# Kernel optimization log

Hardware: AMD Instinct MI355X
Metric: run time of the kernel (lower is better)

The kernel has to match this reference:

```python
import math
import jax, jax.numpy as jnp
import numpy as np

BLOCK = 32          # hard-coded in the CUDA kernels
NUM_HEADS = 16
NUM_BLOCKS = 512    # (max_pos//32) * block_per_row = 128 * 4
DIAG_N = 3
FIRST_N = 0


def _mra2_attention(Q, K, V, mask):
    # Q,K,V: (meta_batch, seq, head_dim); mask: (meta_batch, seq) in {0,1}
    mb, seq_len, d = Q.shape
    bs = BLOCK
    nb = seq_len // bs
    scale = 1.0 / math.sqrt(d)
    Q = Q * mask[:, :, None]
    K = K * mask[:, :, None]
    V = V * mask[:, :, None]

    # ---- low resolution block means (mask-weighted), approx_mode='full' keeps V_hat
    tc = mask.reshape(mb, nb, bs).sum(-1)                 # token count per block
    denom = tc[:, :, None] + 1e-6
    Q_hat = Q.reshape(mb, nb, bs, d).sum(2) / denom       # (mb, nb, d)
    K_hat = K.reshape(mb, nb, bs, d).sum(2) / denom
    V_hat = V.reshape(mb, nb, bs, d).sum(2) / denom
    low_logit = jnp.einsum('bid,bjd->bij', Q_hat, K_hat) * scale
    row_max = low_logit.max(-1, keepdims=True)            # before mask subtraction
    low_logit = low_logit - 10000.0 * ((tc[:, None, :] * tc[:, :, None]) < 0.5).astype(Q.dtype)

    # ---- block index selection (torch runs this under no_grad)
    lrn = jax.lax.stop_gradient(low_logit - row_max)
    if DIAG_N > 0:
        off = DIAG_N // 2
        i = jnp.arange(nb)
        band = (jnp.abs(i[:, None] - i[None, :]) <= off).astype(Q.dtype)
        lrn = lrn + band[None] * 5000.0
    if FIRST_N > 0:
        lrn = lrn.at[:, :FIRST_N, :].add(5000.0)
        lrn = lrn.at[:, :, :FIRST_N].add(5000.0)
    top_vals, indices = jax.lax.top_k(lrn.reshape(mb, nb * nb), NUM_BLOCKS)
    threshold = top_vals.min(-1)
    high_mask = (lrn >= threshold[:, None, None]).astype(Q.dtype)  # selected-block mask

    q_blk = indices // nb                                  # (mb, n) query block ids
    k_blk = indices % nb                                   # (mb, n) key block ids
    Qs = jnp.take_along_axis(Q.reshape(mb, nb, bs, d), q_blk[:, :, None, None], axis=1)
    Ks = jnp.take_along_axis(K.reshape(mb, nb, bs, d), k_blk[:, :, None, None], axis=1)
    Vs = jnp.take_along_axis(V.reshape(mb, nb, bs, d), k_blk[:, :, None, None], axis=1)

    # sampled dense-dense: sparse_C[b,n,k,q] (key-in-block, query-in-block layout as in kernel)
    hi_logit = jnp.einsum('bnkd,bnqd->bnkq', Ks, Qs) * scale

    # per query-row max over selected blocks (kernel index_max; constant for grad)
    b_idx = jnp.arange(mb)[:, None]
    blk_max = hi_logit.max(axis=2)                         # (mb, n, bs) max over key axis
    max_blocks = jnp.full((mb, nb, bs), -1e8, Q.dtype).at[b_idx, q_blk].max(blk_max)
    max_blocks = jax.lax.stop_gradient(max_blocks)
    max_vals = max_blocks.reshape(mb, seq_len)
    max_scatter = jnp.take_along_axis(max_blocks, q_blk[:, :, None], axis=1)[:, :, None, :]

    # key-side mask per selected block (sparse_mask_B)
    mask_blk = jnp.take_along_axis(mask.reshape(mb, nb, bs), k_blk[:, :, None], axis=1)
    hi_attn = jnp.exp(hi_logit - max_scatter - 10000.0 * (1.0 - mask_blk[:, :, :, None]))

    # sparse-dense matmul + reduce-sum normalizer, scattered back per query block
    hi_out = jnp.zeros((mb, nb, bs, d), Q.dtype).at[b_idx, q_blk].add(
        jnp.einsum('bnkq,bnkd->bnqd', hi_attn, Vs)).reshape(mb, seq_len, d)
    hi_norm = jnp.zeros((mb, nb, bs), Q.dtype).at[b_idx, q_blk].add(
        hi_attn.sum(axis=2)).reshape(mb, seq_len)

    # ---- low resolution branch, selected blocks suppressed via high_mask
    low_attn = jnp.exp(low_logit - row_max - 10000.0 * high_mask) * tc[:, None, :]
    low_out = jnp.repeat(jnp.einsum('bij,bjd->bid', low_attn, V_hat), bs, axis=1)
    low_norm = jnp.repeat(low_attn.sum(-1), bs, axis=1)

    log_corr = (jnp.repeat(row_max[:, :, 0], bs, axis=1) - max_vals) * mask
    low_corr = jnp.exp(jnp.minimum(log_corr, 0.0))
    hi_corr = jnp.exp(-jnp.maximum(log_corr, 0.0))

    ctx = hi_out * hi_corr[:, :, None] + low_out * low_corr[:, :, None]
    ctx = ctx / (hi_norm * hi_corr + low_norm * low_corr + 1e-6)[:, :, None]
    return ctx * mask[:, :, None]


def _forward(hidden_states, attention_mask, w_q, b_q, w_k, b_k, w_v, b_v):
    b, s, hdim = hidden_states.shape
    h = NUM_HEADS
    dh = hdim // h

    def split_heads(x):
        return x.reshape(b, s, h, dh).transpose(0, 2, 1, 3).reshape(b * h, s, dh)

    q = split_heads(hidden_states @ w_q.T + b_q)
    k = split_heads(hidden_states @ w_k.T + b_k)
    v = split_heads(hidden_states @ w_v.T + b_v)
    # invert extended additive mask (1 + am/10000) and replicate over heads
    # (torch's .repeat(1, h, 1).reshape(b*h, s) stacks h copies of the [b,s] mask)
    mask = jnp.tile(1.0 + attention_mask / 10000.0, (h, 1))
    ctx = _mra2_attention(q, k, v, mask)
    ctx = ctx.reshape(b, h, s, dh).transpose(0, 2, 1, 3).reshape(b, s, hdim)
    return ctx


def setup_inputs() -> dict:
    key = jax.random.key(0)
    ks = jax.random.split(key, 4)
    H = 1024
    return {
        'hidden_states': jax.random.normal(ks[0], (2, 4096, H), jnp.float32),
        'attention_mask': jnp.zeros((2, 4096), jnp.float32),
        'w_q': jax.random.normal(ks[1], (H, H), jnp.float32) * 0.02,
        'b_q': jnp.zeros((H,), jnp.float32),
        'w_k': jax.random.normal(ks[2], (H, H), jnp.float32) * 0.02,
        'b_k': jnp.zeros((H,), jnp.float32),
        'w_v': jax.random.normal(ks[3], (H, H), jnp.float32) * 0.02,
        'b_v': jnp.zeros((H,), jnp.float32),
    }


def reference(hidden_states, attention_mask, w_q, b_q, w_k, b_k, w_v, b_v):
    return _forward(hidden_states, attention_mask, w_q, b_q, w_k, b_k, w_v, b_v)
```

## Files before the change

kernel.cpp:

```cpp
#include <hip/hip_runtime.h>
#include <cstdint>
#include <cstddef>

#define MAXSEL 160
static constexpr int S    = 4096;
static constexpr int H    = 1024;
static constexpr int DH   = 64;
static constexpr int NB   = 128;
static constexpr int MBH  = 32;
static constexpr int M8   = 8192;
static constexpr int N3   = 3072;

typedef _Float16 half8 __attribute__((ext_vector_type(8)));
typedef _Float16 half4v __attribute__((ext_vector_type(4)));
typedef float floatx4 __attribute__((ext_vector_type(4)));

__device__ __forceinline__ void load_lds16(const void* g, void* l) {
  __builtin_amdgcn_global_load_lds((const __attribute__((address_space(1))) unsigned int*)g,
                                   (__attribute__((address_space(3))) unsigned int*)l,
                                   16, 0, 0);
}

__device__ __forceinline__ int sel8(int t, int4 a, int4 b) {
  int r = a.x;
  r = (t == 1) ? a.y : r;
  r = (t == 2) ? a.z : r;
  r = (t == 3) ? a.w : r;
  r = (t == 4) ? b.x : r;
  r = (t == 5) ? b.y : r;
  r = (t == 6) ? b.z : r;
  r = (t == 7) ? b.w : r;
  return r;
}

__global__ __launch_bounds__(256) void k_prep(const float* __restrict__ hidden,
                                              const float* __restrict__ am,
                                              const float* __restrict__ wq,
                                              const float* __restrict__ wk,
                                              const float* __restrict__ wv,
                                              _Float16* __restrict__ h16,
                                              _Float16* __restrict__ w16,
                                              _Float16* __restrict__ wlo,
                                              _Float16* __restrict__ hb_hi,
                                              _Float16* __restrict__ hb_lo,
                                              float* __restrict__ tcv,
                                              int* __restrict__ selcnt) {
  const int blk_id = blockIdx.x;
  if (blk_id < 256) {
    if (blk_id == 0) {
      for (int i = threadIdx.x; i < MBH * NB; i += 256) selcnt[i] = 0;
    }
    int b2 = blk_id >> 7, blk = blk_id & 127;
    int c = threadIdx.x * 4;
    float4 s0 = make_float4(0.f, 0.f, 0.f, 0.f);
    float4 s1 = make_float4(0.f, 0.f, 0.f, 0.f);
    for (int i = 0; i < 32; i += 4) {
      int pos0 = blk * 32 + i;
      size_t base = ((size_t)b2 * 4096 + pos0) * 1024 + c;
      const float4 x0 = *(const float4*)&hidden[base];
      const float4 x1 = *(const float4*)&hidden[base + 1024];
      const float4 x2 = *(const float4*)&hidden[base + 2048];
      const float4 x3 = *(const float4*)&hidden[base + 3072];
      float a00 = am[pos0],      a01 = am[pos0 + 1],      a02 = am[pos0 + 2],      a03 = am[pos0 + 3];
      float a10 = am[4096+pos0], a11 = am[4096+pos0 + 1], a12 = am[4096+pos0 + 2], a13 = am[4096+pos0 + 3];
      half4v h;
      h[0]=(_Float16)x0.x; h[1]=(_Float16)x0.y; h[2]=(_Float16)x0.z; h[3]=(_Float16)x0.w;
      *(half4v*)&h16[base] = h;
      h[0]=(_Float16)x1.x; h[1]=(_Float16)x1.y; h[2]=(_Float16)x1.z; h[3]=(_Float16)x1.w;
      *(half4v*)&h16[base + 1024] = h;
      h[0]=(_Float16)x2.x; h[1]=(_Float16)x2.y; h[2]=(_Float16)x2.z; h[3]=(_Float16)x2.w;
      *(half4v*)&h16[base + 2048] = h;
      h[0]=(_Float16)x3.x; h[1]=(_Float16)x3.y; h[2]=(_Float16)x3.z; h[3]=(_Float16)x3.w;
      *(half4v*)&h16[base + 3072] = h;
      float m0, m1;
      m0 = 1.f + a00 * 1e-4f; m1 = 1.f + a10 * 1e-4f;
      s0.x += m0*x0.x; s0.y += m0*x0.y; s0.z += m0*x0.z; s0.w += m0*x0.w;
      s1.x += m1*x0.x; s1.y += m1*x0.y; s1.z += m1*x0.z; s1.w += m1*x0.w;
      m0 = 1.f + a01 * 1e-4f; m1 = 1.f + a11 * 1e-4f;
      s0.x += m0*x1.x; s0.y += m0*x1.y; s0.z += m0*x1.z; s0.w += m0*x1.w;
      s1.x += m1*x1.x; s1.y += m1*x1.y; s1.z += m1*x1.z; s1.w += m1*x1.w;
      m0 = 1.f + a02 * 1e-4f; m1 = 1.f + a12 * 1e-4f;
      s0.x += m0*x2.x; s0.y += m0*x2.y; s0.z += m0*x2.z; s0.w += m0*x2.w;
      s1.x += m1*x2.x; s1.y += m1*x2.y; s1.z += m1*x2.z; s1.w += m1*x2.w;
      m0 = 1.f + a03 * 1e-4f; m1 = 1.f + a13 * 1e-4f;
      s0.x += m0*x3.x; s0.y += m0*x3.y; s0.z += m0*x3.z; s0.w += m0*x3.w;
      s1.x += m1*x3.x; s1.y += m1*x3.y; s1.z += m1*x3.z; s1.w += m1*x3.w;
    }
    size_t row0 = (size_t)(b2 * 2 + 0) * 128 + blk;
    size_t row1 = (size_t)(b2 * 2 + 1) * 128 + blk;
    half4v hi, lo;
    hi[0]=(_Float16)s0.x; lo[0]=(_Float16)(s0.x-(float)hi[0]);
    hi[1]=(_Float16)s0.y; lo[1]=(_Float16)(s0.y-(float)hi[1]);
    hi[2]=(_Float16)s0.z; lo[2]=(_Float16)(s0.z-(float)hi[2]);
    hi[3]=(_Float16)s0.w; lo[3]=(_Float16)(s0.w-(float)hi[3]);
    *(half4v*)&hb_hi[row0 * 1024 + c] = hi;
    *(half4v*)&hb_lo[row0 * 1024 + c] = lo;
    hi[0]=(_Float16)s1.x; lo[0]=(_Float16)(s1.x-(float)hi[0]);
    hi[1]=(_Float16)s1.y; lo[1]=(_Float16)(s1.y-(float)hi[1]);
    hi[2]=(_Float16)s1.z; lo[2]=(_Float16)(s1.z-(float)hi[2]);
    hi[3]=(_Float16)s1.w; lo[3]=(_Float16)(s1.w-(float)hi[3]);
    *(half4v*)&hb_hi[row1 * 1024 + c] = hi;
    *(half4v*)&hb_lo[row1 * 1024 + c] = lo;
    if (b2 == 0 && threadIdx.x == 0) {
      float t0 = 0.f, t1 = 0.f;
      for (int i = 0; i < 32; ++i) {
        int pos = blk * 32 + i;
        t0 += 1.f + am[pos] * 1e-4f;
        t1 += 1.f + am[4096 + pos] * 1e-4f;
      }
      tcv[blk] = t0; tcv[128 + blk] = t1;
    }
  } else {
    long j = (long)(blk_id - 256) * 256 + threadIdx.x;
    const long NW4 = (long)H * H / 4;
    int which = (int)(j / NW4);
    long jj = j - (long)which * NW4;
    const float* src = which == 0 ? wq : (which == 1 ? wk : wv);
    float4 x = ((const float4*)src)[jj];
    half4v h;
    h[0] = (_Float16)x.x; h[1] = (_Float16)x.y;
    h[2] = (_Float16)x.z; h[3] = (_Float16)x.w;
    *(half4v*)&w16[j * 4] = h;
    if (which < 2) {
      half4v r;
      r[0] = (_Float16)(x.x - (float)h[0]);
      r[1] = (_Float16)(x.y - (float)h[1]);
      r[2] = (_Float16)(x.z - (float)h[2]);
      r[3] = (_Float16)(x.w - (float)h[3]);
      *(half4v*)&wlo[j * 4] = r;
    }
  }
}

__global__ __launch_bounds__(512, 4) void k_gemm_qkv(const _Float16* __restrict__ A,
                                                     const _Float16* __restrict__ B,
                                                     const float* __restrict__ bq,
                                                     const float* __restrict__ bk,
                                                     const float* __restrict__ bv,
                                                     const float* __restrict__ am,
                                                     _Float16* __restrict__ q16,
                                                     _Float16* __restrict__ k16,
                                                     _Float16* __restrict__ v16,
                                                     const _Float16* __restrict__ Ahi,
                                                     const _Float16* __restrict__ Alo,
                                                     const _Float16* __restrict__ Blo,
                                                     float* __restrict__ sideQK) {
  __shared__ _Float16 sh[36864];

  if (blockIdx.x < 768) {
    const int id = blockIdx.x;
    const int swz = (id & 7) * 96 + (id >> 3);
    const int by = swz / 12;
    const int bx = swz - by * 12;
    const int tid = threadIdx.x;
    const int lane = tid & 63, wv = tid >> 6;
    const int wm = wv >> 2, wn = wv & 3;
    const int l15 = lane & 15, quad = lane >> 4;

    _Float16* As = sh;
    _Float16* Bs = sh + 12288;

    floatx4 acc[4][4] = {};

    const _Float16* Ag = A + (size_t)(by * 128) * 1024;
    const _Float16* Bg = B + (size_t)(bx * 256) * 1024;

    const int gr  = lane >> 2;
    const int gcb = ((lane & 3) ^ ((lane >> 3) & 3)) * 8;
    const _Float16* agl  = Ag + (size_t)(wv * 16 + gr) * 1024 + gcb;
    const _Float16* bgl0 = Bg + (size_t)(wv * 32 + gr) * 1024 + gcb;
    const _Float16* bgl1 = Bg + (size_t)(wv * 32 + 16 + gr) * 1024 + gcb;
    const int aw  = (wv * 16) * 32;
    const int bw0 = (wv * 32) * 32;
    const int bw1 = (wv * 32 + 16) * 32;

#define STAGE(TT, BB)                                                   \
    {                                                                   \
      load_lds16(agl  + (size_t)(TT) * 32, &As[(BB) * 4096 + aw]);      \
      load_lds16(bgl0 + (size_t)(TT) * 32, &Bs[(BB) * 8192 + bw0]);     \
      load_lds16(bgl1 + (size_t)(TT) * 32, &Bs[(BB) * 8192 + bw1]);     \
    }

    STAGE(0, 0)
    STAGE(1, 1)

    const int rc = ((quad ^ ((l15 >> 1) & 3)) << 3);

#pragma unroll
    for (int t = 0; t < 32; ++t) {
      if (t == 31) { asm volatile("s_waitcnt vmcnt(0)" ::: "memory"); }
      else         { asm volatile("s_waitcnt vmcnt(3)" ::: "memory"); }
      __builtin_amdgcn_s_barrier();
      if (t < 30) {
        const int nb = (t + 2) % 3;
        STAGE(t + 2, nb)
      }
      const int bb = t % 3;
      half8 a[4], b[4];
#pragma unroll
      for (int mt = 0; mt < 4; ++mt)
        a[mt] = *(const half8*)&As[bb * 4096 + (wm * 64 + mt * 16 + l15) * 32 + rc];
#pragma unroll
      for (int nt = 0; nt < 4; ++nt)
        b[nt] = *(const half8*)&Bs[bb * 8192 + (wn * 64 + nt * 16 + l15) * 32 + rc];
      __builtin_amdgcn_s_setprio(1);
#pragma unroll
      for (int mt = 0; mt < 4; ++mt)
#pragma unroll
        for (int nt = 0; nt < 4; ++nt)
          acc[mt][nt] = __builtin_amdgcn_mfma_f32_16x16x32_f16(a[mt], b[nt], acc[mt][nt], 0, 0, 0);
      __builtin_amdgcn_s_setprio(0);
    }
#undef STAGE

    const int which = bx >> 2;
    const float* bias = which == 0 ? bq : (which == 1 ? bk : bv);
    _Float16* dst = which == 0 ? q16 : (which == 1 ? k16 : v16);
    const int hh = (bx & 3) * 4 + wn;
    const int m2 = hh & 1;
#pragma unroll
    for (int nt = 0; nt < 4; ++nt) {
      const int dd = nt * 16 + l15;
      const float bsv = bias[hh * 64 + dd];
#pragma unroll
      for (int mt = 0; mt < 4; ++mt) {
#pragma unroll
        for (int r = 0; r < 4; ++r) {
          int srow = by * 128 + wm * 64 + mt * 16 + quad * 4 + r;
          int b2 = srow >> 12, s = srow & 4095;
          float mv = 1.f + am[m2 * 4096 + s] * 1e-4f;
          float v = (acc[mt][nt][r] + bsv) * mv;
          int mb = b2 * 16 + hh;
          dst[((size_t)mb * 4096 + s) * 64 + dd] = (_Float16)v;
        }
      }
    }
    return;
  }

  const int half = threadIdx.x >> 8;
  const int stid = threadIdx.x & 255;
  const int sb   = (blockIdx.x - 768) * 2 + half;
  const int slane = stid & 63, swv = stid >> 6;
  const int kk  = sb >> 8;
  const int sbb = sb & 255;
  const int sbx = sbb & 31;
  const int sby = sbb >> 5;
  const int swm = swv >> 1, swn = swv & 1;
  const int sl15 = slane & 15, squad = slane >> 4;
  _Float16* base = sh + half * 16384;
  _Float16* sAhi = base;
  _Float16* sAlo = base + 4096;
  _Float16* sBhi = base + 8192;
  _Float16* sBlo = base + 12288;

  floatx4 acc[2][2] = {};

  const int srow = slane >> 3;
  const int scol = (((slane & 7) ^ (srow & 7)) * 8);
  const int sswz = sl15 & 7;
  const _Float16* src;
  _Float16* dst;
  if      (swv == 0) { src = Ahi + (size_t)(sby * 64) * 1024; dst = sAhi; }
  else if (swv == 1) { src = Alo + (size_t)(sby * 64) * 1024; dst = sAlo; }
  else if (swv == 2) { src = B   + (size_t)(sbx * 64) * 1024; dst = sBhi; }
  else               { src = Blo + (size_t)(sbx * 64) * 1024; dst = sBlo; }

  const int kbeg = kk * 512;
  for (int k0 = kbeg; k0 < kbeg + 512; k0 += 64) {
    __syncthreads();
#pragma unroll
    for (int i = 0; i < 8; ++i)
      load_lds16(src + (size_t)(i * 8 + srow) * 1024 + k0 + scol, dst + i * 512);
    __syncthreads();
#pragma unroll
    for (int ks = 0; ks < 2; ++ks) {
      const int kc = ks * 4;
      half8 ah[2], al[2], bh[2], bl[2];
#pragma unroll
      for (int mt = 0; mt < 2; ++mt) {
        int off = (swm * 32 + mt * 16 + sl15) * 64 + (((kc + squad) ^ sswz) << 3);
        ah[mt] = *(const half8*)&sAhi[off];
        al[mt] = *(const half8*)&sAlo[off];
      }
#pragma unroll
      for (int nt = 0; nt < 2; ++nt) {
        int off = (swn * 32 + nt * 16 + sl15) * 64 + (((kc + squad) ^ sswz) << 3);
        bh[nt] = *(const half8*)&sBhi[off];
        bl[nt] = *(const half8*)&sBlo[off];
      }
#pragma unroll
      for (int mt = 0; mt < 2; ++mt)
#pragma unroll
        for (int nt = 0; nt < 2; ++nt) {
          acc[mt][nt] = __builtin_amdgcn_mfma_f32_16x16x32_f16(ah[mt], bh[nt], acc[mt][nt], 0, 0, 0);
          acc[mt][nt] = __builtin_amdgcn_mfma_f32_16x16x32_f16(ah[mt], bl[nt], acc[mt][nt], 0, 0, 0);
          acc[mt][nt] = __builtin_amdgcn_mfma_f32_16x16x32_f16(al[mt], bh[nt], acc[mt][nt], 0, 0, 0);
        }
    }
  }
  float* outp = sideQK + (size_t)kk * (512 * 2048);
#pragma unroll
  for (int mt = 0; mt < 2; ++mt)
#pragma unroll
    for (int nt = 0; nt < 2; ++nt)
#pragma unroll
      for (int rr = 0; rr < 4; ++rr) {
        int row = sby * 64 + swm * 32 + mt * 16 + squad * 4 + rr;
        int col = sbx * 64 + swn * 32 + nt * 16 + sl15;
        outp[(size_t)row * 2048 + col] = acc[mt][nt][rr];
      }
}

__global__ __launch_bounds__(256) void k_lowlogit(const float* __restrict__ sideQK,
                                                  const float* __restrict__ tcv,
                                                  const float* __restrict__ bq,
                                                  const float* __restrict__ bk,
                                                  float* __restrict__ ll,
                                                  float* __restrict__ rmaxout,
                                                  const _Float16* __restrict__ v16,
                                                  float* __restrict__ vhat,
                                                  _Float16* __restrict__ v16T) {
  __shared__ __attribute__((aligned(16))) char shraw[37376];
  const int tid = threadIdx.x;

  if (blockIdx.x >= 256) {
    const int lane = tid & 63, wv = tid >> 6;
    _Float16* Vs = (_Float16*)shraw + wv * 2304;
    int bid = (blockIdx.x - 256) * 4 + wv;
    int mb = bid >> 7, blk = bid & 127;
    const _Float16* src = v16 + ((size_t)mb * 4096 + blk * 32) * 64;
    int r = lane >> 3, c = (lane & 7) * 8;
#pragma unroll
    for (int it = 0; it < 4; ++it)
      *(uint4*)&Vs[(it * 8 + r) * 72 + c] = *(const uint4*)&src[(it * 8 + r) * 64 + c];
    __syncthreads();
    float acc = 0.f;
    half8 col[4];
#pragma unroll
    for (int k = 0; k < 32; ++k) {
      _Float16 x = Vs[k * 72 + lane];
      col[k >> 3][k & 7] = x;
      acc += (float)x;
    }
    vhat[(size_t)bid * 64 + lane] = acc / (tcv[(mb & 1) * 128 + blk] + 1e-6f);
    _Float16* dst = v16T + ((size_t)(mb * 128 + blk) * 64 + lane) * 32;
#pragma unroll
    for (int p = 0; p < 4; ++p) *(half8*)&dst[p * 8] = col[p];
    return;
  }

  const int mb = blockIdx.x >> 3;
  const int ib = blockIdx.x & 7;
  const int b2 = mb >> 4, m2 = mb & 1, hh = mb & 15;
  const int combo = b2 * 2 + m2;
  float* Kh  = (float*)shraw;
  float* Qh  = (float*)(shraw + 32768);
  float* tcL = (float*)(shraw + 32768 + 4096);

  const float* P1 = sideQK + (size_t)512 * 2048;

  if (tid < 128) tcL[tid] = tcv[m2 * 128 + tid];
  __syncthreads();
#pragma unroll
  for (int i = 0; i < 8; ++i) {
    int ci = tid + i * 256;
    int row = ci >> 4, c4 = (ci & 15) * 4;
    float tck = tcL[row];
    float den = 1.f / (tck + 1e-6f);
    size_t idx = ((size_t)combo * 128 + row) * 2048 + 1024 + hh * 64 + c4;
    float4 x0 = *(const float4*)&sideQK[idx];
    float4 x1 = *(const float4*)&P1[idx];
    float4 bb = *(const float4*)&bk[hh * 64 + c4];
    float4 o;
    o.x = (x0.x + x1.x + bb.x * tck) * den; o.y = (x0.y + x1.y + bb.y * tck) * den;
    o.z = (x0.z + x1.z + bb.z * tck) * den; o.w = (x0.w + x1.w + bb.w * tck) * den;
    *(float4*)&Kh[row * 64 + c4] = o;
  }
  {
    int row = tid >> 4, c4 = (tid & 15) * 4;
    int gi = ib * 16 + row;
    float tcq = tcL[gi];
    float den = 1.f / (tcq + 1e-6f);
    size_t idx = ((size_t)combo * 128 + gi) * 2048 + hh * 64 + c4;
    float4 x0 = *(const float4*)&sideQK[idx];
    float4 x1 = *(const float4*)&P1[idx];
    float4 bb = *(const float4*)&bq[hh * 64 + c4];
    float4 o;
    o.x = (x0.x + x1.x + bb.x * tcq) * den; o.y = (x0.y + x1.y + bb.y * tcq) * den;
    o.z = (x0.z + x1.z + bb.z * tcq) * den; o.w = (x0.w + x1.w + bb.w * tcq) * den;
    *(float4*)&Qh[row * 64 + c4] = o;
  }
  __syncthreads();

  const int il = tid >> 4, jg = tid & 15;
  const int i = ib * 16 + il;
  float tcq = tcL[i];
  float dots[8] = {};
#pragma unroll
  for (int dd = 0; dd < 16; ++dd) {
    int d4 = ((dd + tid) & 15) * 4;
    float4 qv = *(const float4*)&Qh[il * 64 + d4];
#pragma unroll
    for (int jj = 0; jj < 8; ++jj) {
      float4 kv = *(const float4*)&Kh[(jg * 8 + jj) * 64 + d4];
      dots[jj] += qv.x * kv.x + qv.y * kv.y + qv.z * kv.z + qv.w * kv.w;
    }
  }
  float tmax = -1e30f;
#pragma unroll
  for (int jj = 0; jj < 8; ++jj) {
    int j = jg * 8 + jj;
    float raw = dots[jj] * 0.125f;
    tmax = fmaxf(tmax, raw);
    float pen = (tcq * tcL[j] < 0.5f) ? 10000.f : 0.f;
    ll[(size_t)mb * 16384 + (size_t)i * 128 + j] = raw - pen;
  }
#pragma unroll
  for (int mk = 1; mk < 16; mk <<= 1) tmax = fmaxf(tmax, __shfl_xor(tmax, mk));
  if (jg == 0) rmaxout[mb * 128 + i] = tmax;
}

__global__ __launch_bounds__(256) void k_topk(const float* __restrict__ ll,
                                              const float* __restrict__ rmax,
                                              float* __restrict__ thr,
                                              int* __restrict__ selcnt,
                                              int* __restrict__ selkb) {
  const int mb = blockIdx.x;
  const int t = threadIdx.x;
  const int wid = t >> 6;
  __shared__ int red2[2][4];

  unsigned code[64];
#pragma unroll
  for (int j = 0; j < 64; ++j) {
    int e = j * 256 + t;
    int i = e >> 7, jj = e & 127;
    float lrn = ll[(size_t)mb * 16384 + e] - rmax[mb * 128 + i];
    int di = i - jj;
    if (di <= 1 && di >= -1) lrn += 5000.f;
    unsigned b = __float_as_uint(lrn);
    code[j] = (b & 0x80000000u) ? ~b : (b | 0x80000000u);
  }

  unsigned lo = 0u, hi = 0xFFFFFFFFu;
  for (int it = 0; it < 32; ++it) {
    unsigned mid = lo + ((hi - lo) >> 1);
    int c = 0;
#pragma unroll
    for (int j = 0; j < 64; ++j) c += (code[j] >= mid) ? 1 : 0;
#pragma unroll
    for (int mk = 1; mk < 64; mk <<= 1) c += __shfl_xor(c, mk);
    if ((t & 63) == 0) red2[it & 1][wid] = c;
    __syncthreads();
    int total = red2[it & 1][0] + red2[it & 1][1] + red2[it & 1][2] + red2[it & 1][3];
    if (total >= 512) lo = mid; else hi = mid;
  }
  if (t == 0) {
    unsigned bits = (lo & 0x80000000u) ? (lo & 0x7FFFFFFFu) : ~lo;
    thr[mb] = __uint_as_float(bits);
  }
#pragma unroll
  for (int j = 0; j < 64; ++j) {
    if (code[j] >= lo) {
      int e = j * 256 + t;
      int i = e >> 7, jj = e & 127;
      int slot = atomicAdd(&selcnt[mb * 128 + i], 1);
      if (slot < MAXSEL) selkb[(size_t)(mb * 128 + i) * MAXSEL + slot] = jj;
    }
  }
}

__global__ __launch_bounds__(64) void k_hi(const _Float16* __restrict__ q16,
                                           const _Float16* __restrict__ k16,
                                           const _Float16* __restrict__ v16T,
                                           const int* __restrict__ selcnt,
                                           const int* __restrict__ selkb,
                                           const float* __restrict__ rmax,
                                           const float* __restrict__ thr,
                                           const float* __restrict__ tcv,
                                           const float* __restrict__ vhat,
                                           const float* __restrict__ ll,
                                           const float* __restrict__ am,
                                           float* __restrict__ out) {
  const int mb = blockIdx.x & 31, qb = blockIdx.x >> 5;
  const int sid = mb * 128 + qb;
  const int lane = threadIdx.x;
  const int l15 = lane & 15, quad = lane >> 4;
  const int m2 = mb & 1, b2 = mb >> 4, hh = mb & 15;

  __shared__ _Float16 Ps[32 * 40];

  const _Float16* qbase = q16 + ((size_t)mb * 4096 + qb * 32) * 64;
  half8 aq[2][2];
#pragma unroll
  for (int mt = 0; mt < 2; ++mt)
#pragma unroll
    for (int ks = 0; ks < 2; ++ks)
      aq[mt][ks] = *(const half8*)&qbase[(mt * 16 + l15) * 64 + ks * 32 + quad * 8];

  const int* list = selkb + (size_t)sid * MAXSEL;
  const int4 La = *(const int4*)&list[0];
  const int4 Lb = *(const int4*)&list[4];

  const float rmaxb = rmax[sid];
  const float th = thr[mb];
  const float* llrow = ll + (size_t)mb * 16384 + (size_t)qb * 128;
  const float* tcrow = tcv + m2 * 128;
  const float* vhbase = vhat + ((size_t)(mb * 128)) * 64 + lane;
  float a0 = 0.f, a1 = 0.f, a2 = 0.f, a3 = 0.f;
  float n0 = 0.f, n1 = 0.f, n2 = 0.f, n3 = 0.f;
#pragma unroll 2
  for (int j0 = 0; j0 < 128; j0 += 4) {
    float4 l4 = *(const float4*)&llrow[j0];
    float4 t4 = *(const float4*)&tcrow[j0];
    float v0 = vhbase[(size_t)(j0 + 0) * 64];
    float v1 = vhbase[(size_t)(j0 + 1) * 64];
    float v2 = vhbase[(size_t)(j0 + 2) * 64];
    float v3 = vhbase[(size_t)(j0 + 3) * 64];
    int d0 = qb - j0;
    float lr0 = l4.x - rmaxb + ((d0 <= 1 && d0 >= -1) ? 5000.f : 0.f);
    float lr1 = l4.y - rmaxb + ((d0 <= 2 && d0 >= 0) ? 5000.f : 0.f);
    float lr2 = l4.z - rmaxb + ((d0 <= 3 && d0 >= 1) ? 5000.f : 0.f);
    float lr3 = l4.w - rmaxb + ((d0 <= 4 && d0 >= 2) ? 5000.f : 0.f);
    float w0 = (lr0 >= th) ? 0.f : __expf(l4.x - rmaxb) * t4.x;
    float w1 = (lr1 >= th) ? 0.f : __expf(l4.y - rmaxb) * t4.y;
    float w2 = (lr2 >= th) ? 0.f : __expf(l4.z - rmaxb) * t4.z;
    float w3 = (lr3 >= th) ? 0.f : __expf(l4.w - rmaxb) * t4.w;
    a0 += w0 * v0; a1 += w1 * v1; a2 += w2 * v2; a3 += w3 * v3;
    n0 += w0; n1 += w1; n2 += w2; n3 += w3;
  }
  float accL = (a0 + a1) + (a2 + a3);
  float nrmL = (n0 + n1) + (n2 + n3);

  int nk = selcnt[sid];
  if (nk > MAXSEL) nk = MAXSEL;

  const _Float16* kbase  = k16  + (size_t)mb * 4096 * 64;
  const _Float16* vtbase = v16T + (size_t)mb * 128 * 2048;

  float rm[2][4];
  floatx4 o[2][4] = {};
  floatx4 onrm[2] = {};
#pragma unroll
  for (int mt = 0; mt < 2; ++mt)
#pragma unroll
    for (int r = 0; r < 4; ++r) rm[mt][r] = -1e8f;

  half8 ones;
#pragma unroll
  for (int j = 0; j < 8; ++j) ones[j] = (_Float16)1.f;

  for (int t = 0; t < nk; ++t) {
    const int kb = (t < 8) ? sel8(t, La, Lb) : list[t];
    const _Float16* kp = kbase + (size_t)kb * 32 * 64;
    half8 b0[2], b1[2];
#pragma unroll
    for (int ks = 0; ks < 2; ++ks) {
      b0[ks] = *(const half8*)&kp[(l15) * 64 + ks * 32 + quad * 8];
      b1[ks] = *(const half8*)&kp[(16 + l15) * 64 + ks * 32 + quad * 8];
    }
    const _Float16* vp = vtbase + kb * 2048 + quad * 8;
    half8 vb0 = *(const half8*)&vp[(l15) * 32];
    half8 vb1 = *(const half8*)&vp[(16 + l15) * 32];
    half8 vb2 = *(const half8*)&vp[(32 + l15) * 32];
    half8 vb3 = *(const half8*)&vp[(48 + l15) * 32];

    floatx4 sf[2][2] = {};
    sf[0][0] = __builtin_amdgcn_mfma_f32_16x16x32_f16(aq[0][0], b0[0], sf[0][0], 0, 0, 0);
    sf[0][0] = __builtin_amdgcn_mfma_f32_16x16x32_f16(aq[0][1], b0[1], sf[0][0], 0, 0, 0);
    sf[0][1] = __builtin_amdgcn_mfma_f32_16x16x32_f16(aq[0][0], b1[0], sf[0][1], 0, 0, 0);
    sf[0][1] = __builtin_amdgcn_mfma_f32_16x16x32_f16(aq[0][1], b1[1], sf[0][1], 0, 0, 0);
    sf[1][0] = __builtin_amdgcn_mfma_f32_16x16x32_f16(aq[1][0], b0[0], sf[1][0], 0, 0, 0);
    sf[1][0] = __builtin_amdgcn_mfma_f32_16x16x32_f16(aq[1][1], b0[1], sf[1][0], 0, 0, 0);
    sf[1][1] = __builtin_amdgcn_mfma_f32_16x16x32_f16(aq[1][0], b1[0], sf[1][1], 0, 0, 0);
    sf[1][1] = __builtin_amdgcn_mfma_f32_16x16x32_f16(aq[1][1], b1[1], sf[1][1], 0, 0, 0);

    float pen0, pen1;
    {
      float mk0 = 1.f + am[m2 * 4096 + kb * 32 + l15] * 1e-4f;
      float mk1 = 1.f + am[m2 * 4096 + kb * 32 + 16 + l15] * 1e-4f;
      pen0 = 10000.f * (1.f - mk0);
      pen1 = 10000.f * (1.f - mk1);
    }
#pragma unroll
    for (int mt = 0; mt < 2; ++mt)
#pragma unroll
      for (int r = 0; r < 4; ++r) {
        float s0 = sf[mt][0][r] * 0.125f;
        float s1 = sf[mt][1][r] * 0.125f;
        float v = fmaxf(s0, s1);
#pragma unroll
        for (int mk = 1; mk < 16; mk <<= 1) v = fmaxf(v, __shfl_xor(v, mk));
        float mnew  = fmaxf(rm[mt][r], v);
        float alpha = __expf(rm[mt][r] - mnew);
        rm[mt][r] = mnew;
        float p0 = __expf(s0 - mnew - pen0);
        float p1 = __expf(s1 - mnew - pen1);
        o[mt][0][r] *= alpha; o[mt][1][r] *= alpha;
        o[mt][2][r] *= alpha; o[mt][3][r] *= alpha;
        onrm[mt][r] *= alpha;
        int row = mt * 16 + quad * 4 + r;
        Ps[row * 40 + l15] = (_Float16)p0;
        Ps[row * 40 + 16 + l15] = (_Float16)p1;
      }
    __builtin_amdgcn_sched_barrier(0);
    asm volatile("s_waitcnt lgkmcnt(0)" ::: "memory");
    __builtin_amdgcn_sched_barrier(0);
    half8 pa0 = *(const half8*)&Ps[(l15) * 40 + quad * 8];
    half8 pa1 = *(const half8*)&Ps[(16 + l15) * 40 + quad * 8];
    o[0][0] = __builtin_amdgcn_mfma_f32_16x16x32_f16(pa0, vb0, o[0][0], 0, 0, 0);
    o[0][1] = __builtin_amdgcn_mfma_f32_16x16x32_f16(pa0, vb1, o[0][1], 0, 0, 0);
    o[0][2] = __builtin_amdgcn_mfma_f32_16x16x32_f16(pa0, vb2, o[0][2], 0, 0, 0);
    o[0][3] = __builtin_amdgcn_mfma_f32_16x16x32_f16(pa0, vb3, o[0][3], 0, 0, 0);
    o[1][0] = __builtin_amdgcn_mfma_f32_16x16x32_f16(pa1, vb0, o[1][0], 0, 0, 0);
    o[1][1] = __builtin_amdgcn_mfma_f32_16x16x32_f16(pa1, vb1, o[1][1], 0, 0, 0);
    o[1][2] = __builtin_amdgcn_mfma_f32_16x16x32_f16(pa1, vb2, o[1][2], 0, 0, 0);
    o[1][3] = __builtin_amdgcn_mfma_f32_16x16x32_f16(pa1, vb3, o[1][3], 0, 0, 0);
    onrm[0] = __builtin_amdgcn_mfma_f32_16x16x32_f16(pa0, ones, onrm[0], 0, 0, 0);
    onrm[1] = __builtin_amdgcn_mfma_f32_16x16x32_f16(pa1, ones, onrm[1], 0, 0, 0);
  }

  float lo_d[4];
#pragma unroll
  for (int ntd = 0; ntd < 4; ++ntd) lo_d[ntd] = __shfl(accL, ntd * 16 + l15);
#pragma unroll
  for (int mt = 0; mt < 2; ++mt) {
#pragma unroll
    for (int r = 0; r < 4; ++r) {
      int q = mt * 16 + quad * 4 + r;
      int qpos = qb * 32 + q;
      float mq = 1.f + am[m2 * 4096 + qpos] * 1e-4f;
      float logc = (rmaxb - rm[mt][r]) * mq;
      float lc = __expf(fminf(logc, 0.f));
      float hc = __expf(-fmaxf(logc, 0.f));
      float den = onrm[mt][r] * hc + nrmL * lc + 1e-6f;
      float sc = mq / den;
#pragma unroll
      for (int ntd = 0; ntd < 4; ++ntd) {
        float val = (o[mt][ntd][r] * hc + lo_d[ntd] * lc) * sc;
        out[((size_t)b2 * 4096 + qpos) * 1024 + hh * 64 + ntd * 16 + l15] = val;
      }
    }
  }
}

extern "C" void kernel_launch(void* const* d_in, const int* in_sizes, int n_in,
                              void* d_out, int out_size, void* d_ws, size_t ws_size,
                              hipStream_t stream) {
  const float* hidden = (const float*)d_in[0];
  const float* am     = (const float*)d_in[1];
  const float* wq     = (const float*)d_in[2];
  const float* bq     = (const float*)d_in[3];
  const float* wk     = (const float*)d_in[4];
  const float* bk     = (const float*)d_in[5];
  const float* wv     = (const float*)d_in[6];
  const float* bv     = (const float*)d_in[7];
  float* out = (float*)d_out;

  char* ws = (char*)d_ws;
  size_t off = 0;
  auto alloc = [&](size_t bytes) -> char* {
    char* p = ws + off;
    off += (bytes + 255) & ~(size_t)255;
    return p;
  };
  _Float16* h16    = (_Float16*)alloc((size_t)M8 * H * 2);
  _Float16* w16    = (_Float16*)alloc((size_t)N3 * H * 2);
  _Float16* wlo    = (_Float16*)alloc((size_t)2 * H * H * 2);
  _Float16* q16    = (_Float16*)alloc((size_t)MBH * S * DH * 2);
  _Float16* k16    = (_Float16*)alloc((size_t)MBH * S * DH * 2);
  _Float16* v16    = (_Float16*)alloc((size_t)MBH * S * DH * 2);
  _Float16* hb_hi  = (_Float16*)alloc((size_t)4 * NB * H * 2);
  _Float16* hb_lo  = (_Float16*)alloc((size_t)4 * NB * H * 2);
  float* tcv       = (float*)alloc((size_t)2 * NB * 4);
  float* sideQK    = (float*)alloc((size_t)2 * 512 * 2048 * 4);
  float* ll        = (float*)alloc((size_t)MBH * NB * NB * 4);
  float* rmax      = (float*)alloc((size_t)MBH * NB * 4);
  float* thr       = (float*)alloc((size_t)MBH * 4);
  int*   selcnt    = (int*)alloc((size_t)MBH * NB * 4);
  int*   selkb     = (int*)alloc((size_t)MBH * NB * MAXSEL * 4);
  float* vhat      = (float*)alloc((size_t)MBH * NB * DH * 4);
  _Float16* v16T   = h16;

  k_prep<<<dim3(3328), dim3(256), 0, stream>>>(hidden, am, wq, wk, wv,
                                               h16, w16, wlo, hb_hi, hb_lo, tcv, selcnt);
  k_gemm_qkv<<<dim3(1024), dim3(512), 0, stream>>>(h16, w16, bq, bk, bv, am,
                                                   q16, k16, v16,
                                                   hb_hi, hb_lo, wlo, sideQK);
  k_lowlogit<<<dim3(1280), dim3(256), 0, stream>>>(sideQK, tcv, bq, bk, ll, rmax,
                                                   v16, vhat, v16T);
  k_topk<<<dim3(32), dim3(256), 0, stream>>>(ll, rmax, thr, selcnt, selkb);
  k_hi<<<dim3(4096), dim3(64), 0, stream>>>(q16, k16, v16T, selcnt, selkb, rmax, thr,
                                            tcv, vhat, ll, am, out);
}
```

Baseline: 278.7 us.

## Split k_hi key-block loop across two waves with flash-style merge

k_hi now runs two wavefronts per query block. The waves interleave the selected key blocks and split the low-resolution sweep in half, then merge their running max, output and normaliser through shared memory using a log-sum-exp rescale. The aim is to halve the serial per-block latency and add parallelism per query block. The cost is a shared-memory merge, a barrier and more LDS per block. Each wave handles only about 8 of the roughly 16 selected blocks, so per-wave work becomes small.

```diff
diff --git a/kernel.cpp b/kernel.cpp
--- a/kernel.cpp
+++ b/kernel.cpp
@@ -471,25 +471,27 @@
   }
 }
 
-__global__ __launch_bounds__(64) void k_hi(const _Float16* __restrict__ q16,
-                                           const _Float16* __restrict__ k16,
-                                           const _Float16* __restrict__ v16T,
-                                           const int* __restrict__ selcnt,
-                                           const int* __restrict__ selkb,
-                                           const float* __restrict__ rmax,
-                                           const float* __restrict__ thr,
-                                           const float* __restrict__ tcv,
-                                           const float* __restrict__ vhat,
-                                           const float* __restrict__ ll,
-                                           const float* __restrict__ am,
-                                           float* __restrict__ out) {
+__global__ __launch_bounds__(128) void k_hi(const _Float16* __restrict__ q16,
+                                            const _Float16* __restrict__ k16,
+                                            const _Float16* __restrict__ v16T,
+                                            const int* __restrict__ selcnt,
+                                            const int* __restrict__ selkb,
+                                            const float* __restrict__ rmax,
+                                            const float* __restrict__ thr,
+                                            const float* __restrict__ tcv,
+                                            const float* __restrict__ vhat,
+                                            const float* __restrict__ ll,
+                                            const float* __restrict__ am,
+                                            float* __restrict__ out) {
   const int mb = blockIdx.x & 31, qb = blockIdx.x >> 5;
   const int sid = mb * 128 + qb;
-  const int lane = threadIdx.x;
+  const int tid = threadIdx.x;
+  const int lane = tid & 63, wid = tid >> 6;
   const int l15 = lane & 15, quad = lane >> 4;
   const int m2 = mb & 1, b2 = mb >> 4, hh = mb & 15;
 
-  __shared__ _Float16 Ps[32 * 40];
+  __shared__ _Float16 Ps[2][32 * 40];
+  __shared__ float mrg[64][50];
 
   const _Float16* qbase = q16 + ((size_t)mb * 4096 + qb * 32) * 64;
   half8 aq[2][2];
@@ -511,7 +513,7 @@
   float a0 = 0.f, a1 = 0.f, a2 = 0.f, a3 = 0.f;
   float n0 = 0.f, n1 = 0.f, n2 = 0.f, n3 = 0.f;
 #pragma unroll 2
-  for (int j0 = 0; j0 < 128; j0 += 4) {
+  for (int j0 = wid * 64; j0 < wid * 64 + 64; j0 += 4) {
     float4 l4 = *(const float4*)&llrow[j0];
     float4 t4 = *(const float4*)&tcrow[j0];
     float v0 = vhbase[(size_t)(j0 + 0) * 64];
@@ -551,7 +553,9 @@
 #pragma unroll
   for (int j = 0; j < 8; ++j) ones[j] = (_Float16)1.f;
 
-  for (int t = 0; t < nk; ++t) {
+  _Float16* myPs = &Ps[wid][0];
+
+  for (int t = wid; t < nk; t += 2) {
     const int kb = (t < 8) ? sel8(t, La, Lb) : list[t];
     const _Float16* kp = kbase + (size_t)kb * 32 * 64;
     half8 b0[2], b1[2];
@@ -601,14 +605,14 @@
         o[mt][2][r] *= alpha; o[mt][3][r] *= alpha;
         onrm[mt][r] *= alpha;
         int row = mt * 16 + quad * 4 + r;
-        Ps[row * 40 + l15] = (_Float16)p0;
-        Ps[row * 40 + 16 + l15] = (_Float16)p1;
+        myPs[row * 40 + l15] = (_Float16)p0;
+        myPs[row * 40 + 16 + l15] = (_Float16)p1;
       }
     __builtin_amdgcn_sched_barrier(0);
     asm volatile("s_waitcnt lgkmcnt(0)" ::: "memory");
     __builtin_amdgcn_sched_barrier(0);
-    half8 pa0 = *(const half8*)&Ps[(l15) * 40 + quad * 8];
-    half8 pa1 = *(const half8*)&Ps[(16 + l15) * 40 + quad * 8];
+    half8 pa0 = *(const half8*)&myPs[(l15) * 40 + quad * 8];
+    half8 pa1 = *(const half8*)&myPs[(16 + l15) * 40 + quad * 8];
     o[0][0] = __builtin_amdgcn_mfma_f32_16x16x32_f16(pa0, vb0, o[0][0], 0, 0, 0);
     o[0][1] = __builtin_amdgcn_mfma_f32_16x16x32_f16(pa0, vb1, o[0][1], 0, 0, 0);
     o[0][2] = __builtin_amdgcn_mfma_f32_16x16x32_f16(pa0, vb2, o[0][2], 0, 0, 0);
@@ -619,6 +623,43 @@
     o[1][3] = __builtin_amdgcn_mfma_f32_16x16x32_f16(pa1, vb3, o[1][3], 0, 0, 0);
     onrm[0] = __builtin_amdgcn_mfma_f32_16x16x32_f16(pa0, ones, onrm[0], 0, 0, 0);
     onrm[1] = __builtin_amdgcn_mfma_f32_16x16x32_f16(pa1, ones, onrm[1], 0, 0, 0);
+  }
+
+  if (wid == 1) {
+    float* st = &mrg[lane][0];
+#pragma unroll
+    for (int mt = 0; mt < 2; ++mt)
+#pragma unroll
+      for (int r = 0; r < 4; ++r) {
+#pragma unroll
+        for (int ntd = 0; ntd < 4; ++ntd) st[mt * 16 + ntd * 4 + r] = o[mt][ntd][r];
+        st[32 + mt * 4 + r] = onrm[mt][r];
+        st[40 + mt * 4 + r] = rm[mt][r];
+      }
+    st[48] = accL;
+    st[49] = nrmL;
+  }
+  __syncthreads();
+  if (wid != 0) return;
+
+  {
+    const float* st = &mrg[lane][0];
+    accL += st[48];
+    nrmL += st[49];
+#pragma unroll
+    for (int mt = 0; mt < 2; ++mt)
+#pragma unroll
+      for (int r = 0; r < 4; ++r) {
+        float rmw = st[40 + mt * 4 + r];
+        float mnew = fmaxf(rm[mt][r], rmw);
+        float g0 = __expf(rm[mt][r] - mnew);
+        float g1 = __expf(rmw - mnew);
+        rm[mt][r] = mnew;
+#pragma unroll
+        for (int ntd = 0; ntd < 4; ++ntd)
+          o[mt][ntd][r] = o[mt][ntd][r] * g0 + st[mt * 16 + ntd * 4 + r] * g1;
+        onrm[mt][r] = onrm[mt][r] * g0 + st[32 + mt * 4 + r] * g1;
+      }
   }
 
   float lo_d[4];
@@ -691,6 +732,6 @@
   k_lowlogit<<<dim3(1280), dim3(256), 0, stream>>>(sideQK, tcv, bq, bk, ll, rmax,
                                                    v16, vhat, v16T);
   k_topk<<<dim3(32), dim3(256), 0, stream>>>(ll, rmax, thr, selcnt, selkb);
-  k_hi<<<dim3(4096), dim3(64), 0, stream>>>(q16, k16, v16T, selcnt, selkb, rmax, thr,
-                                            tcv, vhat, ll, am, out);
+  k_hi<<<dim3(4096), dim3(128), 0, stream>>>(q16, k16, v16T, selcnt, selkb, rmax, thr,
+                                             tcv, vhat, ll, am, out);
 }
```

Measured after the change: 294.8 us. 5.8% more time.
